# Kernel optimization log

Hardware: AMD Instinct MI355X
Metric: run time of the kernel (lower is better)

Reference implementation:

```python
import jax, jax.numpy as jnp
import numpy as np

# dims: B batch, L residues, CS=c_s, N_EXP mHC streams, H heads, CH c_hidden,
# PQK/PV qk/v points, CZ=c_p pair channels, RANK z-factor rank, CZQ=CZ//4
B, L, CS, N_EXP, H, CH, PQK, PV, CZ, RANK = 4, 1024, 384, 4, 8, 64, 4, 8, 128, 2
CZQ = CZ // 4
SINKHORN_ITERS = 20


def quat_to_rot(q):
    q = q / jnp.sqrt((q * q).sum(-1, keepdims=True) + 1e-8)
    w, x, y, z = q[..., 0], q[..., 1], q[..., 2], q[..., 3]
    R = jnp.stack([
        1 - 2 * (y * y + z * z), 2 * (x * y - w * z), 2 * (x * z + w * y),
        2 * (x * y + w * z), 1 - 2 * (x * x + z * z), 2 * (y * z - w * x),
        2 * (x * z - w * y), 2 * (y * z + w * x), 1 - 2 * (x * x + y * y)], axis=-1)
    return R.reshape(q.shape[:-1] + (3, 3))


def layer_norm(x, g, b, eps=1e-5):
    mu = x.mean(-1, keepdims=True)
    var = ((x - mu) ** 2).mean(-1, keepdims=True)
    return (x - mu) * jax.lax.rsqrt(var + eps) * g + b


def sinkhorn(logits):
    # project onto doubly-stochastic matrices (Birkhoff polytope), fixed iters
    M = jnp.exp(logits - logits.max(axis=(-2, -1), keepdims=True))
    for _ in range(SINKHORN_ITERS):
        M = M / (M.sum(-1, keepdims=True) + 1e-8)
        M = M / (M.sum(-2, keepdims=True) + 1e-8)
    return M


def _forward(s, z_factor_1, z_factor_2, quat_t, trans, mask, b_pre, b_post, b_res,
             W_pre, W_post, W_res, alpha, Wq, Wk, Wv, Wq_pts, Wk_pts, Wv_pts,
             Wz_q, Wz_k, head_w, Wo, bo, ln1_g, ln1_b, Wt1, bt1, Wt2, bt2,
             Wt3, bt3, lnt_g, lnt_b, Wbb, bbb):
    # --- mHC: expand_input (first layer replicates stream) + dynamic mappings ---
    s_exp = jnp.broadcast_to(s[:, :, None, :], (B, L, N_EXP, CS))
    h = s_exp.reshape(B, L, N_EXP * CS)
    hn = h * jax.lax.rsqrt((h * h).mean(-1, keepdims=True) + 1e-6)
    H_pre = jax.nn.softmax(b_pre + alpha * (hn @ W_pre), -1)        # [B,L,n]
    H_post = 2.0 * jax.nn.sigmoid(b_post + alpha * (hn @ W_post))   # [B,L,n]
    H_res = sinkhorn(b_res + alpha * (hn @ W_res).reshape(B, L, N_EXP, N_EXP))
    s_c = jnp.einsum('bln,blnc->blc', H_pre, s_exp)                 # contraction

    rot = quat_to_rot(quat_t)                                       # [B,L,3,3]

    # --- Flash-IPA (dense math-equivalent reference) ---
    q = (s_c @ Wq).reshape(B, L, H, CH)
    k = (s_c @ Wk).reshape(B, L, H, CH)
    v = (s_c @ Wv).reshape(B, L, H, CH)
    qp = (s_c @ Wq_pts).reshape(B, L, H, PQK, 3)
    kp = (s_c @ Wk_pts).reshape(B, L, H, PQK, 3)
    vp = (s_c @ Wv_pts).reshape(B, L, H, PV, 3)

    def to_global(p):
        return jnp.einsum('blij,blhpj->blhpi', rot, p) + trans[:, :, None, None, :]

    qp_g, kp_g, vp_g = to_global(qp), to_global(kp), to_global(vp)

    # low-rank factorized pair bias (z = outer product of per-residue factors)
    zq = jnp.einsum('blrz,zh->blrh', z_factor_1, Wz_q)
    zk = jnp.einsum('blrz,zh->blrh', z_factor_1, Wz_k)
    bias = jnp.einsum('birh,bjrh->bhij', zq, zk)

    qk = jnp.einsum('bihc,bjhc->bhij', q, k) / np.sqrt(CH)
    qn = (qp_g ** 2).sum((-2, -1)).transpose(0, 2, 1)               # [B,H,L]
    kn = (kp_g ** 2).sum((-2, -1)).transpose(0, 2, 1)
    pdot = jnp.einsum('bihpd,bjhpd->bhij', qp_g, kp_g)
    d2 = qn[:, :, :, None] + kn[:, :, None, :] - 2.0 * pdot         # sum_p ||qp_i - kp_j||^2
    gamma = jax.nn.softplus(head_w)
    wC = np.sqrt(2.0 / (9.0 * PQK))
    wL = np.sqrt(1.0 / 3.0)
    logits = wL * (qk + bias) - (wL * wC * 0.5) * gamma[None, :, None, None] * d2
    logits = jnp.where(mask[:, None, None, :] > 0, logits, -1e9)
    a = jax.nn.softmax(logits, -1)

    o = jnp.einsum('bhij,bjhc->bihc', a, v).reshape(B, L, H * CH)
    opt_g = jnp.einsum('bhij,bjhpd->bihpd', a, vp_g)
    diff = opt_g - trans[:, :, None, None, :]
    opt_l = jnp.einsum('blij,blhpi->blhpj', rot, diff)              # R^T (x - t)
    opt_norm = jnp.sqrt((opt_l ** 2).sum(-1) + 1e-8)
    opair = jnp.einsum('bhij,bjhrc->bihrc', a, z_factor_2).reshape(B, L, H * RANK * CZQ)
    feat = jnp.concatenate([o, opt_l.reshape(B, L, H * PV * 3),
                            opt_norm.reshape(B, L, H * PV), opair], -1)
    ipa_out = feat @ Wo + bo

    # residual + (dropout=identity at eval) + LN + transition (residual MLP) + LN
    s1 = layer_norm(s_c + ipa_out, ln1_g, ln1_b)
    t1 = jax.nn.relu(s1 @ Wt1 + bt1)
    t2 = jax.nn.relu(t1 @ Wt2 + bt2)
    s_ipa = layer_norm(s1 + (t2 @ Wt3 + bt3), lnt_g, lnt_b)

    # backbone update: quaternion (1,b,c,d) + translation, composed with frame
    upd = s_ipa @ Wbb + bbb                                         # [B,L,6]
    quat_u = jnp.concatenate([jnp.ones((B, L, 1), upd.dtype), upd[..., :3]], -1)
    R_u = quat_to_rot(quat_u)
    rot_new = jnp.einsum('blij,bljk->blik', rot, R_u)
    trans_new = jnp.einsum('blij,blj->bli', rot, upd[..., 3:]) + trans

    # mHC combine: H_res @ s  +  H_post^T * s_ipa (broadcast over streams)
    s_out = jnp.einsum('blmn,blnc->blmc', H_res, s_exp) + H_post[..., None] * s_ipa[:, :, None, :]
    return s_out, rot_new, trans_new


def setup_inputs() -> dict:
    key = jax.random.key(0)
    ks = jax.random.split(key, 24)

    def nrm(k, shape, scale=1.0):
        return jax.random.normal(k, shape, jnp.float32) * scale

    FEAT = H * CH + H * PV * 4 + H * RANK * CZQ  # 512 + 256 + 512 = 1280
    return dict(
        s=nrm(ks[0], (B, L, CS)),
        z_factor_1=nrm(ks[1], (B, L, RANK, CZ)),
        z_factor_2=nrm(ks[2], (B, L, H, RANK, CZQ)),
        quat_t=nrm(ks[3], (B, L, 4)),
        trans=nrm(ks[4], (B, L, 3)),
        mask=jnp.ones((B, L), jnp.float32),
        b_pre=nrm(ks[5], (N_EXP,), 0.02),
        b_post=nrm(ks[6], (N_EXP,), 0.02),
        b_res=nrm(ks[7], (N_EXP, N_EXP), 0.02),
        W_pre=nrm(ks[8], (N_EXP * CS, N_EXP), 0.02),
        W_post=nrm(ks[9], (N_EXP * CS, N_EXP), 0.02),
        W_res=nrm(ks[10], (N_EXP * CS, N_EXP * N_EXP), 0.02),
        alpha=jnp.float32(0.01),
        Wq=nrm(ks[11], (CS, H * CH), 0.02),
        Wk=nrm(ks[12], (CS, H * CH), 0.02),
        Wv=nrm(ks[13], (CS, H * CH), 0.02),
        Wq_pts=nrm(ks[14], (CS, H * PQK * 3), 0.02),
        Wk_pts=nrm(ks[15], (CS, H * PQK * 3), 0.02),
        Wv_pts=nrm(ks[16], (CS, H * PV * 3), 0.02),
        Wz_q=nrm(ks[17], (CZ, H), 0.02),
        Wz_k=nrm(ks[18], (CZ, H), 0.02),
        head_w=jnp.zeros((H,), jnp.float32),
        Wo=nrm(ks[19], (FEAT, CS), 0.02),
        bo=jnp.zeros((CS,), jnp.float32),
        ln1_g=jnp.ones((CS,), jnp.float32),
        ln1_b=jnp.zeros((CS,), jnp.float32),
        Wt1=nrm(ks[20], (CS, CS), 0.02),
        bt1=jnp.zeros((CS,), jnp.float32),
        Wt2=nrm(ks[21], (CS, CS), 0.02),
        bt2=jnp.zeros((CS,), jnp.float32),
        Wt3=nrm(ks[22], (CS, CS), 0.02),
        bt3=jnp.zeros((CS,), jnp.float32),
        lnt_g=jnp.ones((CS,), jnp.float32),
        lnt_b=jnp.zeros((CS,), jnp.float32),
        Wbb=nrm(ks[23], (CS, 6), 0.02),
        bbb=jnp.zeros((6,), jnp.float32),
    )


def reference(s, z_factor_1, z_factor_2, quat_t, trans, mask, b_pre, b_post, b_res,
              W_pre, W_post, W_res, alpha, Wq, Wk, Wv, Wq_pts, Wk_pts, Wv_pts,
              Wz_q, Wz_k, head_w, Wo, bo, ln1_g, ln1_b, Wt1, bt1, Wt2, bt2,
              Wt3, bt3, lnt_g, lnt_b, Wbb, bbb):
    return _forward(s, z_factor_1, z_factor_2, quat_t, trans, mask, b_pre, b_post,
                    b_res, W_pre, W_post, W_res, alpha, Wq, Wk, Wv, Wq_pts, Wk_pts,
                    Wv_pts, Wz_q, Wz_k, head_w, Wo, bo, ln1_g, ln1_b, Wt1, bt1,
                    Wt2, bt2, Wt3, bt3, lnt_g, lnt_b, Wbb, bbb)
```

## Files before the change

kernel.cpp:

```cpp
#include <hip/hip_runtime.h>
#include <hip/hip_bf16.h>

typedef __hip_bfloat16 bf16;
typedef float f4v __attribute__((ext_vector_type(4)));
typedef short s8v __attribute__((ext_vector_type(8)));

#define CSD    384
#define LL     1024
#define NH     8
#define BL     4096
#define NPROJ  1920
#define QDP    96
#define VDP    160
#define FEATD  1280

#define OFF_S      0
#define OFF_Z1     1572864
#define OFF_Z2     2621440
#define OFF_QUAT   4718592
#define OFF_TRANS  4734976
#define OFF_MASK   4747264
#define OFF_BPOST  4751360
#define OFF_BRES   4751376
#define OFF_WPOST  4751392
#define OFF_WRES   4757536
#define OFF_ALPHA  4782112
#define OFF_WQ     4782128
#define OFF_WK     4978736
#define OFF_WV     5175344
#define OFF_WQP    5371952
#define OFF_WKP    5408816
#define OFF_WVP    5445680
#define OFF_WZQ    5519408
#define OFF_WZK    5520432
#define OFF_HEADW  5521456
#define OFF_WO     5521472
#define OFF_BO     6012992
#define OFF_LN1G   6013376
#define OFF_LN1B   6013760
#define OFF_WT1    6014144
#define OFF_BT1    6161600
#define OFF_WT2    6161984
#define OFF_BT2    6309440
#define OFF_WT3    6309824
#define OFF_BT3    6457280
#define OFF_LNTG   6457664
#define OFF_LNTB   6458048
#define OFF_WBB    6458432
#define OFF_BBB    6460736
#define IN_END     6460752

#define WS_FLAG    6460752
#define WS_WPOSTR  6460768
#define WS_WRESR   6462304
#define WS_HPOST   6468448
#define WS_ROWSUM  6484832
#define WS_ROTB    6501216
#define WS_WCATT   6538080
#define WS_PROJ    7275360
#define WS_QB      15139680
#define WS_KB      16712544
#define WS_VT      18285408
#define WS_WOT     20906848
#define WS_WT1T    21152608
#define WS_WT2T    21226336
#define WS_WT3T    21300064

#define OUT_ROT 6291456
#define OUT_TR  6328320

#define NSEG 34

struct P36 { const void* p[36]; };

__device__ __forceinline__ float b2f(bf16 x) { return __bfloat162float(x); }

__device__ __forceinline__ short f2bs(float x) {
  unsigned u = __float_as_uint(x);
  u += 0x7FFFu + ((u >> 16) & 1u);
  return (short)(u >> 16);
}

__device__ __forceinline__ float wredf(float v) {
#pragma unroll
  for (int o = 1; o < 64; o <<= 1) v += __shfl_xor(v, o, 64);
  return v;
}

__global__ void detect_k(const unsigned int* __restrict__ mask_raw, int* __restrict__ flag) {
  if (threadIdx.x == 0 && blockIdx.x == 0) flag[0] = (mask_raw[0] == 0x3F803F80u) ? 1 : 0;
}

__global__ __launch_bounds__(256) void cvtall_k(P36 ptrs, float* __restrict__ dst, const int* __restrict__ flagp) {
  const int i = blockIdx.x * 256 + threadIdx.x;
  if (i >= IN_END) return;
  const int flag = flagp[0];
  const int seg_src_t[NSEG] = {0,1,2,3,4,5,7,8,10,11,12,13,14,15,16,17,18,19,20,21,22,23,24,25,26,27,28,29,30,31,32,33,34,35};
  const int seg_dst_t[NSEG] = {OFF_S,OFF_Z1,OFF_Z2,OFF_QUAT,OFF_TRANS,OFF_MASK,OFF_BPOST,OFF_BRES,OFF_WPOST,OFF_WRES,
                               OFF_ALPHA,OFF_WQ,OFF_WK,OFF_WV,OFF_WQP,OFF_WKP,OFF_WVP,OFF_WZQ,OFF_WZK,OFF_HEADW,
                               OFF_WO,OFF_BO,OFF_LN1G,OFF_LN1B,OFF_WT1,OFF_BT1,OFF_WT2,OFF_BT2,OFF_WT3,OFF_BT3,
                               OFF_LNTG,OFF_LNTB,OFF_WBB,OFF_BBB};
  const int seg_cnt_t[NSEG] = {1572864,1048576,2097152,16384,12288,4096,4,16,6144,24576,
                               1,196608,196608,196608,36864,36864,73728,1024,1024,8,
                               491520,384,384,384,147456,384,147456,384,147456,384,
                               384,384,2304,6};
  int off = i, cnt = seg_cnt_t[0];
  const void* sp = ptrs.p[0];
#pragma unroll
  for (int k = 1; k < NSEG; k++) {
    if (i >= seg_dst_t[k]) { off = i - seg_dst_t[k]; cnt = seg_cnt_t[k]; sp = ptrs.p[seg_src_t[k]]; }
  }
  float v = 0.f;
  if (off < cnt) {
    v = flag ? b2f(((const bf16*)sp)[off]) : ((const float*)sp)[off];
  }
  dst[i] = v;
}

__global__ __launch_bounds__(256) void wcatT_k(const float* __restrict__ Wq, const float* __restrict__ Wk,
                                               const float* __restrict__ Wv, const float* __restrict__ Wqp,
                                               const float* __restrict__ Wkp, const float* __restrict__ Wvp,
                                               short* __restrict__ WcatT) {
  int i = blockIdx.x * 256 + threadIdx.x;
  if (i >= CSD * NPROJ) return;
  int k = i / NPROJ, c = i % NPROJ;
  float v;
  if (c < 512)       v = Wq[k * 512 + c];
  else if (c < 1024) v = Wk[k * 512 + c - 512];
  else if (c < 1536) v = Wv[k * 512 + c - 1024];
  else if (c < 1632) v = Wqp[k * 96 + c - 1536];
  else if (c < 1728) v = Wkp[k * 96 + c - 1632];
  else               v = Wvp[k * 192 + c - 1728];
  WcatT[c * CSD + k] = f2bs(v);
}

__global__ __launch_bounds__(256) void wT_k(const float* __restrict__ W, short* __restrict__ Wt, int K, int N) {
  int i = blockIdx.x * 256 + threadIdx.x;
  if (i >= K * N) return;
  int k = i / N, n = i % N;
  Wt[(size_t)n * K + k] = f2bs(W[i]);
}

__global__ __launch_bounds__(256) void wreduce_k(const float* __restrict__ Wpost, const float* __restrict__ Wres,
                                                 float* __restrict__ WpostR, float* __restrict__ WresR) {
  int i = blockIdx.x * 256 + threadIdx.x;
  if (i < CSD * 4) {
    int c = i >> 2, n = i & 3;
    float s = 0.f;
#pragma unroll
    for (int blk = 0; blk < 4; blk++) s += Wpost[(blk * CSD + c) * 4 + n];
    WpostR[i] = s;
  }
  if (i < CSD * 16) {
    int c = i >> 4, n = i & 15;
    float s = 0.f;
#pragma unroll
    for (int blk = 0; blk < 4; blk++) s += Wres[(blk * CSD + c) * 16 + n];
    WresR[i] = s;
  }
}

__global__ __launch_bounds__(64) void mhc_k(const float* __restrict__ sF, const float* __restrict__ quat,
                                            const float* __restrict__ bpost, const float* __restrict__ bres,
                                            const float* __restrict__ alpha_p, const float* __restrict__ WpostR,
                                            const float* __restrict__ WresR, float* __restrict__ hpost,
                                            float* __restrict__ rowsum, float* __restrict__ rotb) {
  const int bl = blockIdx.x, t = threadIdx.x;
  const float* sr = sF + (size_t)bl * CSD;
  float ssq = 0.f, dp[4] = {0.f, 0.f, 0.f, 0.f}, dr[16];
#pragma unroll
  for (int n = 0; n < 16; n++) dr[n] = 0.f;
#pragma unroll
  for (int e = 0; e < 6; e++) {
    const int c = t + e * 64;
    const float sv = sr[c];
    ssq = fmaf(sv, sv, ssq);
#pragma unroll
    for (int n = 0; n < 4; n++) dp[n] = fmaf(sv, WpostR[c * 4 + n], dp[n]);
#pragma unroll
    for (int n = 0; n < 16; n++) dr[n] = fmaf(sv, WresR[c * 16 + n], dr[n]);
  }
  ssq = wredf(ssq);
#pragma unroll
  for (int n = 0; n < 4; n++) dp[n] = wredf(dp[n]);
#pragma unroll
  for (int n = 0; n < 16; n++) dr[n] = wredf(dr[n]);
  const float alpha = alpha_p[0];
  const float invn = rsqrtf(ssq * (1.f / 384.f) + 1e-6f);
  if (t == 0) {
#pragma unroll
    for (int n = 0; n < 4; n++) {
      const float x = bpost[n] + alpha * invn * dp[n];
      hpost[bl * 4 + n] = 2.f / (1.f + __expf(-x));
    }
    float M[16];
    float mx = -1e30f;
#pragma unroll
    for (int k = 0; k < 16; k++) { M[k] = bres[k] + alpha * invn * dr[k]; mx = fmaxf(mx, M[k]); }
#pragma unroll
    for (int k = 0; k < 16; k++) M[k] = __expf(M[k] - mx);
    for (int it = 0; it < 20; it++) {
#pragma unroll
      for (int r = 0; r < 4; r++) {
        const float s4 = M[r * 4] + M[r * 4 + 1] + M[r * 4 + 2] + M[r * 4 + 3];
        const float iv = 1.f / (s4 + 1e-8f);
        M[r * 4] *= iv; M[r * 4 + 1] *= iv; M[r * 4 + 2] *= iv; M[r * 4 + 3] *= iv;
      }
#pragma unroll
      for (int c2 = 0; c2 < 4; c2++) {
        const float s4 = M[c2] + M[4 + c2] + M[8 + c2] + M[12 + c2];
        const float iv = 1.f / (s4 + 1e-8f);
        M[c2] *= iv; M[4 + c2] *= iv; M[8 + c2] *= iv; M[12 + c2] *= iv;
      }
    }
#pragma unroll
    for (int r = 0; r < 4; r++)
      rowsum[bl * 4 + r] = M[r * 4] + M[r * 4 + 1] + M[r * 4 + 2] + M[r * 4 + 3];
  }
  if (t == 1) {
    float w = quat[bl * 4 + 0], x = quat[bl * 4 + 1];
    float y = quat[bl * 4 + 2], z = quat[bl * 4 + 3];
    const float iq = rsqrtf(w * w + x * x + y * y + z * z + 1e-8f);
    w *= iq; x *= iq; y *= iq; z *= iq;
    float* R = rotb + (size_t)bl * 9;
    R[0] = 1.f - 2.f * (y * y + z * z); R[1] = 2.f * (x * y - w * z); R[2] = 2.f * (x * z + w * y);
    R[3] = 2.f * (x * y + w * z); R[4] = 1.f - 2.f * (x * x + z * z); R[5] = 2.f * (y * z - w * x);
    R[6] = 2.f * (x * z - w * y); R[7] = 2.f * (y * z + w * x); R[8] = 1.f - 2.f * (x * x + y * y);
  }
}

__global__ __launch_bounds__(256) void gemm_mfma_k(const float* __restrict__ A, const short* __restrict__ Bt,
                                                   const float* __restrict__ bias, float* __restrict__ C,
                                                   int M, int N, int K, int relu) {
  __shared__ __align__(16) short As[128 * 40];
  __shared__ __align__(16) short Bs[128 * 40];
  const int tid = threadIdx.x;
  const int wid = tid >> 6, lane = tid & 63;
  const int c15 = lane & 15, q = lane >> 4;
  const int bm = blockIdx.y, bn = blockIdx.x;
  const int m_wave = (wid & 1) * 64, n_wave = (wid >> 1) * 64;
  const float* Ab = A + (size_t)(bm * 128) * K;
  const short* Bb = Bt + (size_t)(bn * 128) * K;

  f4v acc[4][4];
#pragma unroll
  for (int mi = 0; mi < 4; mi++)
#pragma unroll
    for (int ni = 0; ni < 4; ni++) acc[mi][ni] = (f4v){0.f, 0.f, 0.f, 0.f};

  for (int k0 = 0; k0 < K; k0 += 32) {
    __syncthreads();
#pragma unroll
    for (int e = 0; e < 4; e++) {
      const int slot = tid + e * 256;
      const int m = slot >> 3, k4 = (slot & 7) * 4;
      const float4 a = *(const float4*)(Ab + (size_t)m * K + k0 + k4);
      short pk[4] = {f2bs(a.x), f2bs(a.y), f2bs(a.z), f2bs(a.w)};
      *(int2*)&As[m * 40 + k4] = *(const int2*)pk;
    }
#pragma unroll
    for (int e = 0; e < 2; e++) {
      const int slot = tid + e * 256;
      const int n = slot >> 2, k8 = (slot & 3) * 8;
      *(int4*)&Bs[n * 40 + k8] = *(const int4*)(Bb + (size_t)n * K + k0 + k8);
    }
    __syncthreads();
    s8v Af[4], Bf[4];
#pragma unroll
    for (int mi = 0; mi < 4; mi++) Af[mi] = *(const s8v*)&As[(m_wave + mi * 16 + c15) * 40 + q * 8];
#pragma unroll
    for (int ni = 0; ni < 4; ni++) Bf[ni] = *(const s8v*)&Bs[(n_wave + ni * 16 + c15) * 40 + q * 8];
#pragma unroll
    for (int mi = 0; mi < 4; mi++)
#pragma unroll
      for (int ni = 0; ni < 4; ni++)
        acc[mi][ni] = __builtin_amdgcn_mfma_f32_16x16x32_bf16(Af[mi], Bf[ni], acc[mi][ni], 0, 0, 0);
  }
#pragma unroll
  for (int mi = 0; mi < 4; mi++) {
#pragma unroll
    for (int r = 0; r < 4; r++) {
      const int row = bm * 128 + m_wave + mi * 16 + q * 4 + r;
      float* Cr = C + (size_t)row * N + bn * 128 + n_wave;
#pragma unroll
      for (int ni = 0; ni < 4; ni++) {
        const int col = bn * 128 + n_wave + ni * 16 + c15;
        float v = acc[mi][ni][r];
        if (bias != nullptr) v += bias[col];
        if (relu) v = fmaxf(v, 0.f);
        Cr[ni * 16 + c15] = v;
      }
    }
  }
}

__global__ __launch_bounds__(256) void assemble_k(const float* __restrict__ proj, const float* __restrict__ rotb,
                                                  const float* __restrict__ trans, const float* __restrict__ z1,
                                                  const float* __restrict__ z2, const float* __restrict__ Wzq,
                                                  const float* __restrict__ Wzk, const float* __restrict__ headw,
                                                  short* __restrict__ Qb, short* __restrict__ Kb,
                                                  short* __restrict__ Vtb) {
  const int idx = blockIdx.x * 256 + threadIdx.x;
  const int h = idx & 7, bl = idx >> 3;
  const float* pr = proj + (size_t)bl * NPROJ;
  const float* R = rotb + (size_t)bl * 9;
  const float txx = trans[bl * 3 + 0], tyy = trans[bl * 3 + 1], tzz = trans[bl * 3 + 2];
  float gamma;
  { const float w = headw[h]; gamma = (w > 20.f) ? w : log1pf(__expf(w)); }
  const float wL = 0.57735026918962576f;
  const float wC = 0.23570226039551584f;
  const float ch = wL * wC * 0.5f * gamma;
  const float qscale = wL * 0.125f;

  float zq0 = 0.f, zq1 = 0.f, zk0 = 0.f, zk1 = 0.f;
  const float* z1r = z1 + (size_t)bl * 256;
  for (int zz = 0; zz < 128; zz++) {
    const float wq = Wzq[zz * 8 + h], wk = Wzk[zz * 8 + h];
    const float a0 = z1r[zz], a1 = z1r[128 + zz];
    zq0 = fmaf(a0, wq, zq0); zq1 = fmaf(a1, wq, zq1);
    zk0 = fmaf(a0, wk, zk0); zk1 = fmaf(a1, wk, zk1);
  }
  const int b = bl >> 10, l = bl & 1023;
  const size_t row = (size_t)(b * NH + h) * LL + l;
  short* Q = Qb + row * QDP;
  short* Kx = Kb + row * QDP;
  for (int c = 0; c < 64; c++) { Q[c] = f2bs(pr[h * 64 + c] * qscale); Kx[c] = f2bs(pr[512 + h * 64 + c]); }
  Q[64] = f2bs(wL * zq0); Q[65] = f2bs(wL * zq1);
  Kx[64] = f2bs(zk0); Kx[65] = f2bs(zk1);
  float qn = 0.f, kn = 0.f;
#pragma unroll
  for (int p = 0; p < 4; p++) {
    const float* pl = pr + 1536 + h * 12 + p * 3;
    float gx = R[0] * pl[0] + R[1] * pl[1] + R[2] * pl[2] + txx;
    float gy = R[3] * pl[0] + R[4] * pl[1] + R[5] * pl[2] + tyy;
    float gz = R[6] * pl[0] + R[7] * pl[1] + R[8] * pl[2] + tzz;
    qn += gx * gx + gy * gy + gz * gz;
    Q[66 + p * 3 + 0] = f2bs(2.f * ch * gx); Q[66 + p * 3 + 1] = f2bs(2.f * ch * gy); Q[66 + p * 3 + 2] = f2bs(2.f * ch * gz);
    const float* pk = pr + 1632 + h * 12 + p * 3;
    gx = R[0] * pk[0] + R[1] * pk[1] + R[2] * pk[2] + txx;
    gy = R[3] * pk[0] + R[4] * pk[1] + R[5] * pk[2] + tyy;
    gz = R[6] * pk[0] + R[7] * pk[1] + R[8] * pk[2] + tzz;
    kn += gx * gx + gy * gy + gz * gz;
    Kx[66 + p * 3 + 0] = f2bs(gx); Kx[66 + p * 3 + 1] = f2bs(gy); Kx[66 + p * 3 + 2] = f2bs(gz);
  }
  Q[78] = f2bs(-ch * qn); Q[79] = f2bs(1.f);
  Kx[78] = f2bs(1.f);     Kx[79] = f2bs(-ch * kn);
  for (int c = 80; c < QDP; c++) { Q[c] = 0; Kx[c] = 0; }
  const size_t vbase = (size_t)(b * NH + h) * VDP * LL + l;
  for (int c = 0; c < 64; c++) Vtb[vbase + (size_t)c * LL] = f2bs(pr[1024 + h * 64 + c]);
#pragma unroll
  for (int p = 0; p < 8; p++) {
    const float* pv = pr + 1728 + h * 24 + p * 3;
    const float gx = R[0] * pv[0] + R[1] * pv[1] + R[2] * pv[2] + txx;
    const float gy = R[3] * pv[0] + R[4] * pv[1] + R[5] * pv[2] + tyy;
    const float gz = R[6] * pv[0] + R[7] * pv[1] + R[8] * pv[2] + tzz;
    Vtb[vbase + (size_t)(64 + p * 3 + 0) * LL] = f2bs(gx);
    Vtb[vbase + (size_t)(64 + p * 3 + 1) * LL] = f2bs(gy);
    Vtb[vbase + (size_t)(64 + p * 3 + 2) * LL] = f2bs(gz);
  }
  const float* z2r = z2 + ((size_t)bl * NH + h) * 64;
  for (int c = 0; c < 64; c++) Vtb[vbase + (size_t)(88 + c) * LL] = f2bs(z2r[c]);
  for (int c = 152; c < VDP; c++) Vtb[vbase + (size_t)c * LL] = 0;
}

__global__ __launch_bounds__(256) void attn_k(const short* __restrict__ Qb, const short* __restrict__ Kb,
                                              const short* __restrict__ Vtb, const float* __restrict__ maskF,
                                              float* __restrict__ Oext) {
  __shared__ __align__(16) short Ks[32 * 104];
  __shared__ __align__(16) short Vs[160 * 40];
  __shared__ __align__(16) short Ps[4 * 16 * 40];
  __shared__ float Msl[32];
  const int tid = threadIdx.x;
  const int wid = tid >> 6;
  const int lane = tid & 63;
  const int c15 = lane & 15;
  const int q = lane >> 4;
  const int bh = blockIdx.y;
  const int b = bh >> 3, h = bh & 7;
  const int i0 = blockIdx.x * 64 + wid * 16;

  s8v Qa[3];
  const short* Qrow = Qb + ((size_t)bh * LL + i0 + c15) * QDP;
#pragma unroll
  for (int kc = 0; kc < 3; kc++) Qa[kc] = *(const s8v*)(Qrow + kc * 32 + q * 8);

  f4v Of[10];
#pragma unroll
  for (int vt = 0; vt < 10; vt++) Of[vt] = (f4v){0.f, 0.f, 0.f, 0.f};
  float mold[4] = {-1e30f, -1e30f, -1e30f, -1e30f};
  float lsum[4] = {0.f, 0.f, 0.f, 0.f};

  const short* Kbase = Kb + (size_t)bh * LL * QDP;
  const short* Vbase = Vtb + (size_t)bh * VDP * LL;
  short* Pl = Ps + wid * 640;

  for (int jt = 0; jt < 32; jt++) {
    const int j0 = jt * 32;
    __syncthreads();
    for (int u = tid; u < 384; u += 256) {
      const int r = u / 12, cc = u % 12;
      *(int4*)&Ks[r * 104 + cc * 8] = *(const int4*)(Kbase + (size_t)(j0 + r) * QDP + cc * 8);
    }
    for (int u = tid; u < 640; u += 256) {
      const int cc = u >> 2, part = u & 3;
      *(int4*)&Vs[cc * 40 + part * 8] = *(const int4*)(Vbase + (size_t)cc * LL + j0 + part * 8);
    }
    if (tid < 32) Msl[tid] = maskF[b * LL + j0 + tid];
    __syncthreads();

    f4v Sf0 = (f4v){0.f, 0.f, 0.f, 0.f}, Sf1 = (f4v){0.f, 0.f, 0.f, 0.f};
#pragma unroll
    for (int kc = 0; kc < 3; kc++) {
      const s8v K0 = *(const s8v*)&Ks[c15 * 104 + kc * 32 + q * 8];
      const s8v K1 = *(const s8v*)&Ks[(16 + c15) * 104 + kc * 32 + q * 8];
      Sf0 = __builtin_amdgcn_mfma_f32_16x16x32_bf16(Qa[kc], K0, Sf0, 0, 0, 0);
      Sf1 = __builtin_amdgcn_mfma_f32_16x16x32_bf16(Qa[kc], K1, Sf1, 0, 0, 0);
    }
    const float mv0 = Msl[c15], mv1 = Msl[16 + c15];
    float lg0[4], lg1[4], tm[4], al[4], p0[4], p1[4];
#pragma unroll
    for (int r = 0; r < 4; r++) {
      lg0[r] = (mv0 > 0.f) ? Sf0[r] : -1e9f;
      lg1[r] = (mv1 > 0.f) ? Sf1[r] : -1e9f;
      tm[r] = fmaxf(lg0[r], lg1[r]);
    }
#pragma unroll
    for (int r = 0; r < 4; r++) {
      tm[r] = fmaxf(tm[r], __shfl_xor(tm[r], 1, 64));
      tm[r] = fmaxf(tm[r], __shfl_xor(tm[r], 2, 64));
      tm[r] = fmaxf(tm[r], __shfl_xor(tm[r], 4, 64));
      tm[r] = fmaxf(tm[r], __shfl_xor(tm[r], 8, 64));
    }
#pragma unroll
    for (int r = 0; r < 4; r++) {
      const float mn = fmaxf(mold[r], tm[r]);
      al[r] = __expf(mold[r] - mn);
      mold[r] = mn;
      p0[r] = __expf(lg0[r] - mn);
      p1[r] = __expf(lg1[r] - mn);
      lsum[r] = lsum[r] * al[r] + p0[r] + p1[r];
    }
#pragma unroll
    for (int vt = 0; vt < 10; vt++) {
#pragma unroll
      for (int r = 0; r < 4; r++) Of[vt][r] *= al[r];
    }
#pragma unroll
    for (int r = 0; r < 4; r++) {
      Pl[(q * 4 + r) * 40 + c15] = f2bs(p0[r]);
      Pl[(q * 4 + r) * 40 + 16 + c15] = f2bs(p1[r]);
    }
    __syncthreads();
    const s8v Pa = *(const s8v*)&Pl[c15 * 40 + q * 8];
#pragma unroll
    for (int vt = 0; vt < 10; vt++) {
      const s8v Vf = *(const s8v*)&Vs[(vt * 16 + c15) * 40 + q * 8];
      Of[vt] = __builtin_amdgcn_mfma_f32_16x16x32_bf16(Pa, Vf, Of[vt], 0, 0, 0);
    }
  }
#pragma unroll
  for (int r = 0; r < 4; r++) {
    lsum[r] += __shfl_xor(lsum[r], 1, 64);
    lsum[r] += __shfl_xor(lsum[r], 2, 64);
    lsum[r] += __shfl_xor(lsum[r], 4, 64);
    lsum[r] += __shfl_xor(lsum[r], 8, 64);
  }
#pragma unroll
  for (int r = 0; r < 4; r++) {
    const float inv = 1.f / lsum[r];
    const int i = i0 + q * 4 + r;
    float* Or = Oext + ((size_t)(b * LL + i) * NH + h) * VDP;
#pragma unroll
    for (int vt = 0; vt < 10; vt++) Or[vt * 16 + c15] = Of[vt][r] * inv;
  }
}

__global__ __launch_bounds__(256) void feat_k(const float* __restrict__ Oext, const float* __restrict__ rotb,
                                              const float* __restrict__ trans, float* __restrict__ feat) {
  const int idx = blockIdx.x * 256 + threadIdx.x;
  const int h = idx & 7, bl = idx >> 3;
  const float* O = Oext + (size_t)(bl * 8 + h) * VDP;
  float* f = feat + (size_t)bl * FEATD;
  for (int c = 0; c < 64; c++) f[h * 64 + c] = O[c];
  const float* R = rotb + (size_t)bl * 9;
  const float txx = trans[bl * 3 + 0], tyy = trans[bl * 3 + 1], tzz = trans[bl * 3 + 2];
#pragma unroll
  for (int p = 0; p < 8; p++) {
    const float dx = O[64 + p * 3 + 0] - txx;
    const float dy = O[64 + p * 3 + 1] - tyy;
    const float dz = O[64 + p * 3 + 2] - tzz;
    const float lx = R[0] * dx + R[3] * dy + R[6] * dz;
    const float ly = R[1] * dx + R[4] * dy + R[7] * dz;
    const float lz = R[2] * dx + R[5] * dy + R[8] * dz;
    f[512 + h * 24 + p * 3 + 0] = lx;
    f[512 + h * 24 + p * 3 + 1] = ly;
    f[512 + h * 24 + p * 3 + 2] = lz;
    f[704 + h * 8 + p] = sqrtf(lx * lx + ly * ly + lz * lz + 1e-8f);
  }
  for (int c = 0; c < 64; c++) f[768 + h * 64 + c] = O[88 + c];
}

__global__ __launch_bounds__(64) void ln_k(const float* __restrict__ x, const float* __restrict__ resid,
                                           const float* __restrict__ g, const float* __restrict__ bta,
                                           float* __restrict__ out) {
  const int row = blockIdx.x, t = threadIdx.x;
  const float* xr = x + (size_t)row * CSD;
  const float* rr = resid + (size_t)row * CSD;
  float v[6];
  float s = 0.f;
#pragma unroll
  for (int e = 0; e < 6; e++) {
    const int c = t + e * 64;
    v[e] = xr[c] + rr[c];
    s += v[e];
  }
  s = wredf(s);
  const float mu = s * (1.f / 384.f);
  float var = 0.f;
#pragma unroll
  for (int e = 0; e < 6; e++) { const float d = v[e] - mu; var = fmaf(d, d, var); }
  var = wredf(var) * (1.f / 384.f);
  const float inv = rsqrtf(var + 1e-5f);
#pragma unroll
  for (int e = 0; e < 6; e++) {
    const int c = t + e * 64;
    out[(size_t)row * CSD + c] = (v[e] - mu) * inv * g[c] + bta[c];
  }
}

__global__ __launch_bounds__(64) void final_k(const float* __restrict__ sF, const float* __restrict__ sipa,
                                              const float* __restrict__ rotb, const float* __restrict__ trans,
                                              const float* __restrict__ hpost, const float* __restrict__ rowsum,
                                              const float* __restrict__ Wbb, const float* __restrict__ bbb,
                                              const int* __restrict__ flagp, void* __restrict__ outv) {
  const int bl = blockIdx.x, t = threadIdx.x;
  const int flag = flagp[0];
  bf16* outb = (bf16*)outv;
  float* outf = (float*)outv;
  const float* si = sipa + (size_t)bl * CSD;
  float d6[6] = {0.f, 0.f, 0.f, 0.f, 0.f, 0.f};
#pragma unroll
  for (int e = 0; e < 6; e++) {
    const int c = t + e * 64;
    const float v = si[c];
#pragma unroll
    for (int u = 0; u < 6; u++) d6[u] = fmaf(v, Wbb[c * 6 + u], d6[u]);
  }
#pragma unroll
  for (int u = 0; u < 6; u++) d6[u] = wredf(d6[u]);
  float upd[6];
#pragma unroll
  for (int u = 0; u < 6; u++) upd[u] = d6[u] + bbb[u];
  const float* R = rotb + (size_t)bl * 9;
  if (t == 0) {
    float w = 1.f, x = upd[0], y = upd[1], z = upd[2];
    const float iq = rsqrtf(w * w + x * x + y * y + z * z + 1e-8f);
    w *= iq; x *= iq; y *= iq; z *= iq;
    const float Ru[9] = {1.f - 2.f * (y * y + z * z), 2.f * (x * y - w * z), 2.f * (x * z + w * y),
                         2.f * (x * y + w * z), 1.f - 2.f * (x * x + z * z), 2.f * (y * z - w * x),
                         2.f * (x * z - w * y), 2.f * (y * z + w * x), 1.f - 2.f * (x * x + y * y)};
#pragma unroll
    for (int i = 0; i < 3; i++)
#pragma unroll
      for (int j = 0; j < 3; j++) {
        const float rv = R[i * 3 + 0] * Ru[0 + j] + R[i * 3 + 1] * Ru[3 + j] + R[i * 3 + 2] * Ru[6 + j];
        const size_t o = OUT_ROT + (size_t)bl * 9 + i * 3 + j;
        if (flag) outb[o] = __float2bfloat16(rv); else outf[o] = rv;
      }
#pragma unroll
    for (int i = 0; i < 3; i++) {
      const float tv = R[i * 3 + 0] * upd[3] + R[i * 3 + 1] * upd[4] + R[i * 3 + 2] * upd[5] + trans[bl * 3 + i];
      const size_t o = OUT_TR + (size_t)bl * 3 + i;
      if (flag) outb[o] = __float2bfloat16(tv); else outf[o] = tv;
    }
  }
  const float hp0 = hpost[bl * 4 + 0], hp1 = hpost[bl * 4 + 1], hp2 = hpost[bl * 4 + 2], hp3 = hpost[bl * 4 + 3];
  const float rs0 = rowsum[bl * 4 + 0], rs1 = rowsum[bl * 4 + 1], rs2 = rowsum[bl * 4 + 2], rs3 = rowsum[bl * 4 + 3];
  const float* sr = sF + (size_t)bl * CSD;
#pragma unroll
  for (int e = 0; e < 6; e++) {
    const int c = t + e * 64;
    const float sv = sr[c], sp = si[c];
    const size_t base = (size_t)bl * 4 * CSD + c;
    const float o0 = rs0 * sv + hp0 * sp;
    const float o1 = rs1 * sv + hp1 * sp;
    const float o2 = rs2 * sv + hp2 * sp;
    const float o3 = rs3 * sv + hp3 * sp;
    if (flag) {
      outb[base + 0 * CSD] = __float2bfloat16(o0);
      outb[base + 1 * CSD] = __float2bfloat16(o1);
      outb[base + 2 * CSD] = __float2bfloat16(o2);
      outb[base + 3 * CSD] = __float2bfloat16(o3);
    } else {
      outf[base + 0 * CSD] = o0;
      outf[base + 1 * CSD] = o1;
      outf[base + 2 * CSD] = o2;
      outf[base + 3 * CSD] = o3;
    }
  }
}

extern "C" void kernel_launch(void* const* d_in, const int* in_sizes, int n_in,
                              void* d_out, int out_size, void* d_ws, size_t ws_size,
                              hipStream_t stream) {
  float* ws = (float*)d_ws;
  int* flag = (int*)(ws + WS_FLAG);

  P36 ptrs;
  for (int i = 0; i < 36; i++) ptrs.p[i] = d_in[i];

  float* sF     = ws + OFF_S;
  float* WpostR = ws + WS_WPOSTR;
  float* WresR  = ws + WS_WRESR;
  float* hpost  = ws + WS_HPOST;
  float* rowsum = ws + WS_ROWSUM;
  float* rotb   = ws + WS_ROTB;
  short* WcatT  = (short*)(ws + WS_WCATT);
  short* WoT    = (short*)(ws + WS_WOT);
  short* Wt1T   = (short*)(ws + WS_WT1T);
  short* Wt2T   = (short*)(ws + WS_WT2T);
  short* Wt3T   = (short*)(ws + WS_WT3T);
  float* proj   = ws + WS_PROJ;
  short* Qb     = (short*)(ws + WS_QB);
  short* Kb     = (short*)(ws + WS_KB);
  short* Vtb    = (short*)(ws + WS_VT);
  float* Oext   = ws + WS_PROJ;
  float* featb  = ws + WS_QB;
  float* x1s1   = ws + WS_PROJ;
  float* t1b    = ws + WS_QB;
  float* t2b    = ws + WS_KB;
  float* x3     = ws + WS_PROJ + 1572864;
  float* sipa   = ws + WS_KB;

  detect_k<<<1, 64, 0, stream>>>((const unsigned int*)d_in[5], flag);
  cvtall_k<<<(IN_END + 255) / 256, 256, 0, stream>>>(ptrs, ws, flag);
  wcatT_k<<<2880, 256, 0, stream>>>(ws + OFF_WQ, ws + OFF_WK, ws + OFF_WV,
                                    ws + OFF_WQP, ws + OFF_WKP, ws + OFF_WVP, WcatT);
  wT_k<<<1920, 256, 0, stream>>>(ws + OFF_WO, WoT, FEATD, CSD);
  wT_k<<<576, 256, 0, stream>>>(ws + OFF_WT1, Wt1T, CSD, CSD);
  wT_k<<<576, 256, 0, stream>>>(ws + OFF_WT2, Wt2T, CSD, CSD);
  wT_k<<<576, 256, 0, stream>>>(ws + OFF_WT3, Wt3T, CSD, CSD);
  wreduce_k<<<24, 256, 0, stream>>>(ws + OFF_WPOST, ws + OFF_WRES, WpostR, WresR);
  mhc_k<<<BL, 64, 0, stream>>>(sF, ws + OFF_QUAT, ws + OFF_BPOST, ws + OFF_BRES, ws + OFF_ALPHA,
                               WpostR, WresR, hpost, rowsum, rotb);
  gemm_mfma_k<<<dim3(15, 32), 256, 0, stream>>>(sF, WcatT, nullptr, proj, BL, NPROJ, CSD, 0);
  assemble_k<<<128, 256, 0, stream>>>(proj, rotb, ws + OFF_TRANS, ws + OFF_Z1, ws + OFF_Z2,
                                      ws + OFF_WZQ, ws + OFF_WZK, ws + OFF_HEADW, Qb, Kb, Vtb);
  attn_k<<<dim3(16, 32), 256, 0, stream>>>(Qb, Kb, Vtb, ws + OFF_MASK, Oext);
  feat_k<<<128, 256, 0, stream>>>(Oext, rotb, ws + OFF_TRANS, featb);
  gemm_mfma_k<<<dim3(3, 32), 256, 0, stream>>>(featb, WoT, ws + OFF_BO, x1s1, BL, CSD, FEATD, 0);
  ln_k<<<BL, 64, 0, stream>>>(x1s1, sF, ws + OFF_LN1G, ws + OFF_LN1B, x1s1);
  gemm_mfma_k<<<dim3(3, 32), 256, 0, stream>>>(x1s1, Wt1T, ws + OFF_BT1, t1b, BL, CSD, CSD, 1);
  gemm_mfma_k<<<dim3(3, 32), 256, 0, stream>>>(t1b, Wt2T, ws + OFF_BT2, t2b, BL, CSD, CSD, 1);
  gemm_mfma_k<<<dim3(3, 32), 256, 0, stream>>>(t2b, Wt3T, ws + OFF_BT3, x3, BL, CSD, CSD, 0);
  ln_k<<<BL, 64, 0, stream>>>(x3, x1s1, ws + OFF_LNTG, ws + OFF_LNTB, sipa);
  final_k<<<BL, 64, 0, stream>>>(sF, sipa, rotb, ws + OFF_TRANS, hpost, rowsum,
                                 ws + OFF_WBB, ws + OFF_BBB, flag, d_out);
}
```

Measured before the change: 543.7 us.

## Split attention KV range across wave halves, vectorize assemble stores, add V transpose

The attention kernel now uses 512-thread blocks where two groups of four waves each process half of the key range for the same query tile. Their partial softmax states are merged through shared memory at the end, and a per-wave barrier is removed. The rescale of the output accumulator is skipped when no row maximum increases. The assemble kernel now writes Q, K and row-major V as packed int4 bf16 stores, and a new transpose kernel produces the column-major V layout. Together these target the strided scalar stores in assemble and the limited parallelism and occupancy in attention, at the cost of an extra kernel launch and extra workspace traffic.

After: 542.4 us. No clear change (-0.2%).

```diff
diff --git a/kernel.cpp b/kernel.cpp
--- a/kernel.cpp
+++ b/kernel.cpp
@@ -65,6 +65,7 @@
 #define WS_WT1T    21152608
 #define WS_WT2T    21226336
 #define WS_WT3T    21300064
+#define WS_VROW    21373792
 
 #define OUT_ROT 6291456
 #define OUT_TR  6328320
@@ -79,6 +80,10 @@
   unsigned u = __float_as_uint(x);
   u += 0x7FFFu + ((u >> 16) & 1u);
   return (short)(u >> 16);
+}
+
+__device__ __forceinline__ int packbf(float lo, float hi) {
+  return (int)(unsigned short)f2bs(lo) | ((int)f2bs(hi) << 16);
 }
 
 __device__ __forceinline__ float wredf(float v) {
@@ -298,8 +303,8 @@
                                                   const float* __restrict__ trans, const float* __restrict__ z1,
                                                   const float* __restrict__ z2, const float* __restrict__ Wzq,
                                                   const float* __restrict__ Wzk, const float* __restrict__ headw,
-                                                  short* __restrict__ Qb, short* __restrict__ Kb,
-                                                  short* __restrict__ Vtb) {
+                                                  int* __restrict__ Qo4, int* __restrict__ Ko4,
+                                                  int* __restrict__ Vr4) {
   const int idx = blockIdx.x * 256 + threadIdx.x;
   const int h = idx & 7, bl = idx >> 3;
   const float* pr = proj + (size_t)bl * NPROJ;
@@ -322,11 +327,24 @@
   }
   const int b = bl >> 10, l = bl & 1023;
   const size_t row = (size_t)(b * NH + h) * LL + l;
-  short* Q = Qb + row * QDP;
-  short* Kx = Kb + row * QDP;
-  for (int c = 0; c < 64; c++) { Q[c] = f2bs(pr[h * 64 + c] * qscale); Kx[c] = f2bs(pr[512 + h * 64 + c]); }
-  Q[64] = f2bs(wL * zq0); Q[65] = f2bs(wL * zq1);
-  Kx[64] = f2bs(zk0); Kx[65] = f2bs(zk1);
+  int* Qo = Qo4 + row * 48;
+  int* Ko = Ko4 + row * 48;
+  int* Vo = Vr4 + row * 80;
+#pragma unroll
+  for (int g = 0; g < 8; g++) {
+    int4 qi, ki, vi;
+#pragma unroll
+    for (int t2 = 0; t2 < 4; t2++) {
+      const int c = g * 8 + t2 * 2;
+      ((int*)&qi)[t2] = packbf(pr[h * 64 + c] * qscale, pr[h * 64 + c + 1] * qscale);
+      ((int*)&ki)[t2] = packbf(pr[512 + h * 64 + c], pr[512 + h * 64 + c + 1]);
+      ((int*)&vi)[t2] = packbf(pr[1024 + h * 64 + c], pr[1024 + h * 64 + c + 1]);
+    }
+    ((int4*)Qo)[g] = qi; ((int4*)Ko)[g] = ki; ((int4*)Vo)[g] = vi;
+  }
+  float qt16[16], kt16[16];
+  qt16[0] = wL * zq0; qt16[1] = wL * zq1;
+  kt16[0] = zk0; kt16[1] = zk1;
   float qn = 0.f, kn = 0.f;
 #pragma unroll
   for (int p = 0; p < 4; p++) {
@@ -335,49 +353,99 @@
     float gy = R[3] * pl[0] + R[4] * pl[1] + R[5] * pl[2] + tyy;
     float gz = R[6] * pl[0] + R[7] * pl[1] + R[8] * pl[2] + tzz;
     qn += gx * gx + gy * gy + gz * gz;
-    Q[66 + p * 3 + 0] = f2bs(2.f * ch * gx); Q[66 + p * 3 + 1] = f2bs(2.f * ch * gy); Q[66 + p * 3 + 2] = f2bs(2.f * ch * gz);
+    qt16[2 + p * 3 + 0] = 2.f * ch * gx; qt16[2 + p * 3 + 1] = 2.f * ch * gy; qt16[2 + p * 3 + 2] = 2.f * ch * gz;
     const float* pk = pr + 1632 + h * 12 + p * 3;
     gx = R[0] * pk[0] + R[1] * pk[1] + R[2] * pk[2] + txx;
     gy = R[3] * pk[0] + R[4] * pk[1] + R[5] * pk[2] + tyy;
     gz = R[6] * pk[0] + R[7] * pk[1] + R[8] * pk[2] + tzz;
     kn += gx * gx + gy * gy + gz * gz;
-    Kx[66 + p * 3 + 0] = f2bs(gx); Kx[66 + p * 3 + 1] = f2bs(gy); Kx[66 + p * 3 + 2] = f2bs(gz);
-  }
-  Q[78] = f2bs(-ch * qn); Q[79] = f2bs(1.f);
-  Kx[78] = f2bs(1.f);     Kx[79] = f2bs(-ch * kn);
-  for (int c = 80; c < QDP; c++) { Q[c] = 0; Kx[c] = 0; }
-  const size_t vbase = (size_t)(b * NH + h) * VDP * LL + l;
-  for (int c = 0; c < 64; c++) Vtb[vbase + (size_t)c * LL] = f2bs(pr[1024 + h * 64 + c]);
+    kt16[2 + p * 3 + 0] = gx; kt16[2 + p * 3 + 1] = gy; kt16[2 + p * 3 + 2] = gz;
+  }
+  qt16[14] = -ch * qn; qt16[15] = 1.f;
+  kt16[14] = 1.f;      kt16[15] = -ch * kn;
+#pragma unroll
+  for (int g = 0; g < 2; g++) {
+    int4 qi, ki;
+#pragma unroll
+    for (int t2 = 0; t2 < 4; t2++) {
+      const int c = g * 8 + t2 * 2;
+      ((int*)&qi)[t2] = packbf(qt16[c], qt16[c + 1]);
+      ((int*)&ki)[t2] = packbf(kt16[c], kt16[c + 1]);
+    }
+    ((int4*)Qo)[8 + g] = qi; ((int4*)Ko)[8 + g] = ki;
+  }
+  int4 z4; z4.x = 0; z4.y = 0; z4.z = 0; z4.w = 0;
+  ((int4*)Qo)[10] = z4; ((int4*)Qo)[11] = z4;
+  ((int4*)Ko)[10] = z4; ((int4*)Ko)[11] = z4;
+  float vt24[24];
 #pragma unroll
   for (int p = 0; p < 8; p++) {
     const float* pv = pr + 1728 + h * 24 + p * 3;
-    const float gx = R[0] * pv[0] + R[1] * pv[1] + R[2] * pv[2] + txx;
-    const float gy = R[3] * pv[0] + R[4] * pv[1] + R[5] * pv[2] + tyy;
-    const float gz = R[6] * pv[0] + R[7] * pv[1] + R[8] * pv[2] + tzz;
-    Vtb[vbase + (size_t)(64 + p * 3 + 0) * LL] = f2bs(gx);
-    Vtb[vbase + (size_t)(64 + p * 3 + 1) * LL] = f2bs(gy);
-    Vtb[vbase + (size_t)(64 + p * 3 + 2) * LL] = f2bs(gz);
+    vt24[p * 3 + 0] = R[0] * pv[0] + R[1] * pv[1] + R[2] * pv[2] + txx;
+    vt24[p * 3 + 1] = R[3] * pv[0] + R[4] * pv[1] + R[5] * pv[2] + tyy;
+    vt24[p * 3 + 2] = R[6] * pv[0] + R[7] * pv[1] + R[8] * pv[2] + tzz;
+  }
+#pragma unroll
+  for (int g = 0; g < 3; g++) {
+    int4 vi;
+#pragma unroll
+    for (int t2 = 0; t2 < 4; t2++) {
+      const int c = g * 8 + t2 * 2;
+      ((int*)&vi)[t2] = packbf(vt24[c], vt24[c + 1]);
+    }
+    ((int4*)Vo)[8 + g] = vi;
   }
   const float* z2r = z2 + ((size_t)bl * NH + h) * 64;
-  for (int c = 0; c < 64; c++) Vtb[vbase + (size_t)(88 + c) * LL] = f2bs(z2r[c]);
-  for (int c = 152; c < VDP; c++) Vtb[vbase + (size_t)c * LL] = 0;
-}
-
-__global__ __launch_bounds__(256) void attn_k(const short* __restrict__ Qb, const short* __restrict__ Kb,
-                                              const short* __restrict__ Vtb, const float* __restrict__ maskF,
-                                              float* __restrict__ Oext) {
-  __shared__ __align__(16) short Ks[32 * 104];
-  __shared__ __align__(16) short Vs[160 * 40];
-  __shared__ __align__(16) short Ps[4 * 16 * 40];
-  __shared__ float Msl[32];
+#pragma unroll
+  for (int g = 0; g < 8; g++) {
+    int4 vi;
+#pragma unroll
+    for (int t2 = 0; t2 < 4; t2++) {
+      const int c = g * 8 + t2 * 2;
+      ((int*)&vi)[t2] = packbf(z2r[c], z2r[c + 1]);
+    }
+    ((int4*)Vo)[11 + g] = vi;
+  }
+  ((int4*)Vo)[19] = z4;
+}
+
+__global__ __launch_bounds__(256) void vtrans_k(const short* __restrict__ Vrow, short* __restrict__ Vtb) {
+  __shared__ __align__(16) short T[64 * 168];
   const int tid = threadIdx.x;
-  const int wid = tid >> 6;
-  const int lane = tid & 63;
-  const int c15 = lane & 15;
-  const int q = lane >> 4;
   const int bh = blockIdx.y;
+  const int l0 = blockIdx.x * 64;
+  const short* src = Vrow + (size_t)bh * LL * VDP + (size_t)l0 * VDP;
+  for (int u = tid; u < 1280; u += 256) {
+    const int ll = u / 20, j = u % 20;
+    *(int4*)&T[ll * 168 + j * 8] = *(const int4*)(src + (size_t)ll * VDP + j * 8);
+  }
+  __syncthreads();
+  short* dst = Vtb + (size_t)bh * VDP * LL + l0;
+  for (int u = tid; u < 1280; u += 256) {
+    const int c = u >> 3, seg = u & 7;
+    short tmp[8];
+#pragma unroll
+    for (int e = 0; e < 8; e++) tmp[e] = T[(seg * 8 + e) * 168 + c];
+    *(int4*)(dst + (size_t)c * LL + seg * 8) = *(const int4*)tmp;
+  }
+}
+
+__global__ __launch_bounds__(512, 4) void attn_k(const short* __restrict__ Qb, const short* __restrict__ Kb,
+                                                 const short* __restrict__ Vtb, const float* __restrict__ maskF,
+                                                 float* __restrict__ Oext) {
+  __shared__ __align__(16) short smem[24704];
+  short* Ks = smem;
+  short* Vs = smem + 6656;
+  short* Ps = smem + 19456;
+  float* Msl = (float*)(smem + 24576);
+  const int tid = threadIdx.x;
+  const int wid = tid >> 6, lane = tid & 63;
+  const int c15 = lane & 15, q = lane >> 4;
+  const int blk = blockIdx.x;
+  const int bh = blk & 31, qt = blk >> 5;
   const int b = bh >> 3, h = bh & 7;
-  const int i0 = blockIdx.x * 64 + wid * 16;
+  const int half = wid >> 2, mw = wid & 3;
+  const int i0 = qt * 64 + mw * 16;
 
   s8v Qa[3];
   const short* Qrow = Qb + ((size_t)bh * LL + i0 + c15) * QDP;
@@ -392,32 +460,39 @@
 
   const short* Kbase = Kb + (size_t)bh * LL * QDP;
   const short* Vbase = Vtb + (size_t)bh * VDP * LL;
+  short* Ksl = Ks + half * 3328;
+  short* Vsl = Vs + half * 6400;
   short* Pl = Ps + wid * 640;
-
-  for (int jt = 0; jt < 32; jt++) {
+  const float* Msw = Msl + half * 32;
+
+  for (int jt = 0; jt < 16; jt++) {
     const int j0 = jt * 32;
     __syncthreads();
-    for (int u = tid; u < 384; u += 256) {
-      const int r = u / 12, cc = u % 12;
-      *(int4*)&Ks[r * 104 + cc * 8] = *(const int4*)(Kbase + (size_t)(j0 + r) * QDP + cc * 8);
-    }
-    for (int u = tid; u < 640; u += 256) {
-      const int cc = u >> 2, part = u & 3;
-      *(int4*)&Vs[cc * 40 + part * 8] = *(const int4*)(Vbase + (size_t)cc * LL + j0 + part * 8);
-    }
-    if (tid < 32) Msl[tid] = maskF[b * LL + j0 + tid];
+    for (int u = tid; u < 768; u += 512) {
+      const int hs = u / 384, v2 = u - hs * 384;
+      const int rr = v2 / 12, cc = v2 % 12;
+      *(int4*)&Ks[hs * 3328 + rr * 104 + cc * 8] =
+          *(const int4*)(Kbase + (size_t)(hs * 512 + j0 + rr) * QDP + cc * 8);
+    }
+    for (int u = tid; u < 1280; u += 512) {
+      const int hs = u / 640, v2 = u - hs * 640;
+      const int cc = v2 >> 2, part = v2 & 3;
+      *(int4*)&Vs[hs * 6400 + cc * 40 + part * 8] =
+          *(const int4*)(Vbase + (size_t)cc * LL + hs * 512 + j0 + part * 8);
+    }
+    if (tid < 64) Msl[tid] = maskF[b * LL + (tid >> 5) * 512 + j0 + (tid & 31)];
     __syncthreads();
 
     f4v Sf0 = (f4v){0.f, 0.f, 0.f, 0.f}, Sf1 = (f4v){0.f, 0.f, 0.f, 0.f};
 #pragma unroll
     for (int kc = 0; kc < 3; kc++) {
-      const s8v K0 = *(const s8v*)&Ks[c15 * 104 + kc * 32 + q * 8];
-      const s8v K1 = *(const s8v*)&Ks[(16 + c15) * 104 + kc * 32 + q * 8];
+      const s8v K0 = *(const s8v*)&Ksl[c15 * 104 + kc * 32 + q * 8];
+      const s8v K1 = *(const s8v*)&Ksl[(16 + c15) * 104 + kc * 32 + q * 8];
       Sf0 = __builtin_amdgcn_mfma_f32_16x16x32_bf16(Qa[kc], K0, Sf0, 0, 0, 0);
       Sf1 = __builtin_amdgcn_mfma_f32_16x16x32_bf16(Qa[kc], K1, Sf1, 0, 0, 0);
     }
-    const float mv0 = Msl[c15], mv1 = Msl[16 + c15];
-    float lg0[4], lg1[4], tm[4], al[4], p0[4], p1[4];
+    const float mv0 = Msw[c15], mv1 = Msw[16 + c15];
+    float lg0[4], lg1[4], tm[4], p0[4], p1[4];
 #pragma unroll
     for (int r = 0; r < 4; r++) {
       lg0[r] = (mv0 > 0.f) ? Sf0[r] : -1e9f;
@@ -431,30 +506,40 @@
       tm[r] = fmaxf(tm[r], __shfl_xor(tm[r], 4, 64));
       tm[r] = fmaxf(tm[r], __shfl_xor(tm[r], 8, 64));
     }
-#pragma unroll
-    for (int r = 0; r < 4; r++) {
-      const float mn = fmaxf(mold[r], tm[r]);
-      al[r] = __expf(mold[r] - mn);
-      mold[r] = mn;
-      p0[r] = __expf(lg0[r] - mn);
-      p1[r] = __expf(lg1[r] - mn);
-      lsum[r] = lsum[r] * al[r] + p0[r] + p1[r];
-    }
-#pragma unroll
-    for (int vt = 0; vt < 10; vt++) {
-#pragma unroll
-      for (int r = 0; r < 4; r++) Of[vt][r] *= al[r];
+    const bool need = (tm[0] > mold[0]) | (tm[1] > mold[1]) | (tm[2] > mold[2]) | (tm[3] > mold[3]);
+    if (__any(need)) {
+      float al[4];
+#pragma unroll
+      for (int r = 0; r < 4; r++) {
+        const float mn = fmaxf(mold[r], tm[r]);
+        al[r] = __expf(mold[r] - mn);
+        mold[r] = mn;
+        p0[r] = __expf(lg0[r] - mn);
+        p1[r] = __expf(lg1[r] - mn);
+        lsum[r] = lsum[r] * al[r] + p0[r] + p1[r];
+      }
+#pragma unroll
+      for (int vt = 0; vt < 10; vt++) {
+#pragma unroll
+        for (int r = 0; r < 4; r++) Of[vt][r] *= al[r];
+      }
+    } else {
+#pragma unroll
+      for (int r = 0; r < 4; r++) {
+        p0[r] = __expf(lg0[r] - mold[r]);
+        p1[r] = __expf(lg1[r] - mold[r]);
+        lsum[r] += p0[r] + p1[r];
+      }
     }
 #pragma unroll
     for (int r = 0; r < 4; r++) {
       Pl[(q * 4 + r) * 40 + c15] = f2bs(p0[r]);
       Pl[(q * 4 + r) * 40 + 16 + c15] = f2bs(p1[r]);
     }
-    __syncthreads();
     const s8v Pa = *(const s8v*)&Pl[c15 * 40 + q * 8];
 #pragma unroll
     for (int vt = 0; vt < 10; vt++) {
-      const s8v Vf = *(const s8v*)&Vs[(vt * 16 + c15) * 40 + q * 8];
+      const s8v Vf = *(const s8v*)&Vsl[(vt * 16 + c15) * 40 + q * 8];
       Of[vt] = __builtin_amdgcn_mfma_f32_16x16x32_bf16(Pa, Vf, Of[vt], 0, 0, 0);
     }
   }
@@ -465,13 +550,34 @@
     lsum[r] += __shfl_xor(lsum[r], 4, 64);
     lsum[r] += __shfl_xor(lsum[r], 8, 64);
   }
-#pragma unroll
-  for (int r = 0; r < 4; r++) {
-    const float inv = 1.f / lsum[r];
-    const int i = i0 + q * 4 + r;
-    float* Or = Oext + ((size_t)(b * LL + i) * NH + h) * VDP;
-#pragma unroll
-    for (int vt = 0; vt < 10; vt++) Or[vt * 16 + c15] = Of[vt][r] * inv;
+  float* Obuf = (float*)smem;
+  float* Mbuf = (float*)(smem + 20480);
+  float* Lbuf = Mbuf + 64;
+  __syncthreads();
+  if (half == 1) {
+#pragma unroll
+    for (int r = 0; r < 4; r++) {
+      const int rowi = mw * 16 + q * 4 + r;
+#pragma unroll
+      for (int vt = 0; vt < 10; vt++) Obuf[rowi * 160 + vt * 16 + c15] = Of[vt][r];
+      if (c15 == 0) { Mbuf[rowi] = mold[r]; Lbuf[rowi] = lsum[r]; }
+    }
+  }
+  __syncthreads();
+  if (half == 0) {
+#pragma unroll
+    for (int r = 0; r < 4; r++) {
+      const int rowi = mw * 16 + q * 4 + r;
+      const float m2 = Mbuf[rowi], l2 = Lbuf[rowi];
+      const float mx = fmaxf(mold[r], m2);
+      const float a1 = __expf(mold[r] - mx), a2 = __expf(m2 - mx);
+      const float inv = 1.f / (lsum[r] * a1 + l2 * a2);
+      const int i = i0 + q * 4 + r;
+      float* Or = Oext + ((size_t)(b * LL + i) * NH + h) * VDP;
+#pragma unroll
+      for (int vt = 0; vt < 10; vt++)
+        Or[vt * 16 + c15] = (Of[vt][r] * a1 + Obuf[rowi * 160 + vt * 16 + c15] * a2) * inv;
+    }
   }
 }
 
@@ -624,6 +730,7 @@
   short* Qb     = (short*)(ws + WS_QB);
   short* Kb     = (short*)(ws + WS_KB);
   short* Vtb    = (short*)(ws + WS_VT);
+  short* Vrow   = (short*)(ws + WS_VROW);
   float* Oext   = ws + WS_PROJ;
   float* featb  = ws + WS_QB;
   float* x1s1   = ws + WS_PROJ;
@@ -645,8 +752,10 @@
                                WpostR, WresR, hpost, rowsum, rotb);
   gemm_mfma_k<<<dim3(15, 32), 256, 0, stream>>>(sF, WcatT, nullptr, proj, BL, NPROJ, CSD, 0);
   assemble_k<<<128, 256, 0, stream>>>(proj, rotb, ws + OFF_TRANS, ws + OFF_Z1, ws + OFF_Z2,
-                                      ws + OFF_WZQ, ws + OFF_WZK, ws + OFF_HEADW, Qb, Kb, Vtb);
-  attn_k<<<dim3(16, 32), 256, 0, stream>>>(Qb, Kb, Vtb, ws + OFF_MASK, Oext);
+                                      ws + OFF_WZQ, ws + OFF_WZK, ws + OFF_HEADW,
+                                      (int*)Qb, (int*)Kb, (int*)Vrow);
+  vtrans_k<<<dim3(16, 32), 256, 0, stream>>>(Vrow, Vtb);
+  attn_k<<<512, 512, 0, stream>>>(Qb, Kb, Vtb, ws + OFF_MASK, Oext);
   feat_k<<<128, 256, 0, stream>>>(Oext, rotb, ws + OFF_TRANS, featb);
   gemm_mfma_k<<<dim3(3, 32), 256, 0, stream>>>(featb, WoT, ws + OFF_BO, x1s1, BL, CSD, FEATD, 0);
   ln_k<<<BL, 64, 0, stream>>>(x1s1, sF, ws + OFF_LN1G, ws + OFF_LN1B, x1s1);
```
